# Performance work log

Hardware: AMD Instinct MI355X
Metric: run time of the kernel (lower is better)

The kernel has to match this reference:

```python
import jax, jax.numpy as jnp
import numpy as np
from jax import lax

D_MODEL, D_INNER, D_CONV, DT_RANK, D_STATE = 1024, 2048, 4, 64, 16
B_SZ, L = 1, 2048
EPS = 1e-5


def setup_inputs() -> dict:
    key = jax.random.key(0)
    ks = jax.random.split(key, 10)
    s = 0.02
    return {
        "x": jax.random.normal(ks[0], (B_SZ, L, D_MODEL), dtype=jnp.float32),
        "W_in": jax.random.normal(ks[1], (2 * D_INNER, D_MODEL), dtype=jnp.float32) * s,
        "conv_w": jax.random.normal(ks[2], (D_INNER, D_CONV), dtype=jnp.float32) * 0.1,
        "conv_b": jnp.zeros((D_INNER,), dtype=jnp.float32),
        "W_xproj": jax.random.normal(ks[3], (DT_RANK + 2 * D_STATE, D_INNER), dtype=jnp.float32) * s,
        "W_dt": jax.random.normal(ks[4], (D_INNER, DT_RANK), dtype=jnp.float32) * s,
        "b_dt": jnp.zeros((D_INNER,), dtype=jnp.float32),
        "A_log": jnp.broadcast_to(jnp.log(jnp.arange(1, D_STATE + 1, dtype=jnp.float32)), (D_INNER, D_STATE)).copy(),
        "D": jnp.ones((D_INNER,), dtype=jnp.float32),
        "W_out": jax.random.normal(ks[5], (D_MODEL, D_INNER), dtype=jnp.float32) * s,
        "norm_w": jnp.ones((D_MODEL,), dtype=jnp.float32),
    }


def _mamba_block(xn, W_in, conv_w, conv_b, W_xproj, W_dt, b_dt, A_log, D, W_out):
    b, l, _ = xn.shape
    # in_proj -> split into x branch and gate (res) branch
    xz = jnp.einsum("bld,ed->ble", xn, W_in)  # (b, l, 2*d_inner)
    xc, res = jnp.split(xz, 2, axis=-1)
    # depthwise causal conv1d over time (padding=d_conv-1, trimmed to l)
    xp = jnp.pad(xc, ((0, 0), (D_CONV - 1, 0), (0, 0)))
    conv = conv_b
    acc = jnp.zeros_like(xc)
    for k in range(D_CONV):
        acc = acc + xp[:, k:k + l, :] * conv_w[:, k]
    xs = jax.nn.silu(acc + conv_b)  # (b, l, d_inner)
    # x_proj -> delta (low-rank), B, C
    dbc = jnp.einsum("bld,ed->ble", xs, W_xproj)
    dt, Bm, Cm = jnp.split(dbc, [DT_RANK, DT_RANK + D_STATE], axis=-1)
    delta = jax.nn.softplus(jnp.einsum("blr,dr->bld", dt, W_dt) + b_dt)  # (b,l,d_inner)
    A = -jnp.exp(A_log)  # (d_inner, d_state)
    # discretize
    deltaA = jnp.exp(jnp.einsum("bld,dn->bldn", delta, A))
    dBu = jnp.einsum("bld,bln,bld->bldn", delta, Bm, xs)
    # selective scan over time
    def step(h, inp):
        dA_t, dBu_t, C_t = inp
        h = dA_t * h + dBu_t                      # (b, d_inner, d_state)
        y_t = jnp.einsum("bdn,bn->bd", h, C_t)
        return h, y_t
    h0 = jnp.zeros((b, D_INNER, D_STATE), dtype=xs.dtype)
    _, ys = lax.scan(step, h0, (deltaA.transpose(1, 0, 2, 3), dBu.transpose(1, 0, 2, 3), Cm.transpose(1, 0, 2)))
    y = ys.transpose(1, 0, 2) + xs * D  # (b, l, d_inner)
    y = y * jax.nn.silu(res)            # gate
    return jnp.einsum("bld,ed->ble", y, W_out)


def reference(x, W_in, conv_w, conv_b, W_xproj, W_dt, b_dt, A_log, D, W_out, norm_w):
    # RMSNorm
    xn = x * jax.lax.rsqrt(jnp.mean(x * x, axis=-1, keepdims=True) + EPS) * norm_w
    # Mamba mixer + residual
    return _mamba_block(xn, W_in, conv_w, conv_b, W_xproj, W_dt, b_dt, A_log, D, W_out) + x
```

## Files before the change

kernel.cpp:

```cpp
#include <hip/hip_runtime.h>
#include <hip/hip_bf16.h>

#define D_MODEL 1024
#define D_INNER 2048
#define DT_RANK 64
#define D_STATE 16
#define LSEQ    2048
#define CHUNK   32
#define NCHUNK  (LSEQ / CHUNK)
#define DN      (D_INNER * D_STATE)
#define KSPL_O  4
#define KSPL_X  16

typedef __attribute__((ext_vector_type(8))) short  short8;
typedef __attribute__((ext_vector_type(4))) float  float4v;
typedef __hip_bfloat16 bf16;

static __device__ __forceinline__ float b2f(bf16 v) { return __bfloat162float(v); }
static __device__ __forceinline__ bf16  f2b(float v) { return __float2bfloat16(v); }
static __device__ __forceinline__ float us2f(unsigned short u) {
    union { unsigned int i; float f; } cc; cc.i = ((unsigned int)u) << 16; return cc.f;
}
static __device__ __forceinline__ unsigned short f2us(float v) {
    return __bfloat16_as_ushort(__float2bfloat16(v));
}

#define GLOAD_LDS16(g, l)                                                          \
    __builtin_amdgcn_global_load_lds((const __attribute__((address_space(1))) void*)(g), \
                                     (__attribute__((address_space(3))) void*)(l), 16, 0, 0)

#define N1 (2 * D_INNER * D_MODEL)
#define N2 (D_MODEL * D_INNER)
#define N3 (96 * D_INNER)
#define N4 (D_INNER * DT_RANK)
#define NCAST4 ((N1 + N2 + N3 + N4) / 4)
__global__ __launch_bounds__(256)
void prep_kernel(const float* __restrict__ x, const float* __restrict__ nw,
                 bf16* __restrict__ xn,
                 const float* __restrict__ w_in, const float* __restrict__ w_out,
                 const float* __restrict__ w_xp, const float* __restrict__ w_dt,
                 bf16* __restrict__ o_in, bf16* __restrict__ o_out,
                 bf16* __restrict__ o_xp, bf16* __restrict__ o_dt) {
    int t = threadIdx.x;
    if (blockIdx.x < LSEQ) {
        int l = blockIdx.x;
        float4v v = ((const float4v*)(x + (size_t)l * D_MODEL))[t];
        float ssq = v[0]*v[0] + v[1]*v[1] + v[2]*v[2] + v[3]*v[3];
        for (int o = 32; o > 0; o >>= 1) ssq += __shfl_down(ssq, o);
        __shared__ float part[4];
        int lane = t & 63, wid = t >> 6;
        if (lane == 0) part[wid] = ssq;
        __syncthreads();
        float tot = part[0] + part[1] + part[2] + part[3];
        float sc = rsqrtf(tot * (1.0f / D_MODEL) + 1e-5f);
        float4v nv = ((const float4v*)nw)[t];
        bf16* op = xn + (size_t)l * D_MODEL + t * 4;
        op[0] = f2b(v[0] * sc * nv[0]);
        op[1] = f2b(v[1] * sc * nv[1]);
        op[2] = f2b(v[2] * sc * nv[2]);
        op[3] = f2b(v[3] * sc * nv[3]);
        return;
    }
    int i4 = (blockIdx.x - LSEQ) * 256 + t;
    if (i4 >= NCAST4) return;
    const float* src; bf16* dst; int base;
    if (i4 < N1 / 4)                { src = w_in;  dst = o_in;  base = 0; }
    else if (i4 < (N1 + N2) / 4)    { src = w_out; dst = o_out; base = N1 / 4; }
    else if (i4 < (N1+N2+N3) / 4)   { src = w_xp;  dst = o_xp;  base = (N1+N2) / 4; }
    else                            { src = w_dt;  dst = o_dt;  base = (N1+N2+N3) / 4; }
    int j = i4 - base;
    float4v v = ((const float4v*)src)[j];
    bf16* o = dst + j * 4;
    o[0] = f2b(v[0]); o[1] = f2b(v[1]); o[2] = f2b(v[2]); o[3] = f2b(v[3]);
}

template <int MODE>
__global__ __launch_bounds__(512)
void gemm_fast(const bf16* __restrict__ Ab, const bf16* __restrict__ Bb,
               int M, int N, int K, int kLen,
               float* __restrict__ outF, bf16* __restrict__ outB,
               const float* __restrict__ bias) {
    __shared__ short As[2][128 * 64];
    __shared__ short Bs[2][128 * 64];
    const short* Ap = (const short*)Ab;
    const short* Bp = (const short*)Bb;

    int t = threadIdx.x;
    int lane = t & 63, wid = t >> 6;

    int bx, by, bz;
    if (MODE == 0) {
        int id = blockIdx.y * gridDim.x + blockIdx.x;
        int xcd = id & 7, slot = id >> 3;
        bx = (xcd & 3) * 8 + (slot & 7);
        by = (xcd >> 2) * 8 + (slot >> 3);
        bz = 0;
    } else if (MODE == 4) {
        int id = (blockIdx.z * gridDim.y + blockIdx.y) * gridDim.x + blockIdx.x;
        int xcd = id & 7, slot = id >> 3;
        bx = slot % gridDim.x;
        int byz = xcd * ((gridDim.y * gridDim.z) / 8) + slot / gridDim.x;
        by = byz % gridDim.y;
        bz = byz / gridDim.y;
    } else {
        bx = blockIdx.x; by = blockIdx.y; bz = blockIdx.z;
    }
    int mBase = by * 128, nBase = bx * 128;
    int kBase = bz * kLen;
    int wm = 32 * (wid >> 1), wn = 64 * (wid & 1);
    int lr = lane & 15, quad = lane >> 4;

    int srow = 16 * wid + (lane >> 3);
    int cg2 = (lane & 7) ^ (lane >> 3);
    const short* gA = Ap + (size_t)(mBase + srow) * K + cg2 * 8;
    const short* gB = Bp + (size_t)(nBase + srow) * K + cg2 * 8;

    float4v acc[2][4] = {};

    #pragma unroll
    for (int g = 0; g < 2; ++g) {
        GLOAD_LDS16(gA + (size_t)g * 8 * K + kBase, &As[0][(16 * wid + g * 8) * 64]);
        GLOAD_LDS16(gB + (size_t)g * 8 * K + kBase, &Bs[0][(16 * wid + g * 8) * 64]);
    }

    int p = 0;
    for (int kt = kBase; kt < kBase + kLen; kt += 64, p ^= 1) {
        __syncthreads();
        if (kt + 64 < kBase + kLen) {
            int kn = kt + 64, q = p ^ 1;
            #pragma unroll
            for (int g = 0; g < 2; ++g) {
                GLOAD_LDS16(gA + (size_t)g * 8 * K + kn, &As[q][(16 * wid + g * 8) * 64]);
                GLOAD_LDS16(gB + (size_t)g * 8 * K + kn, &Bs[q][(16 * wid + g * 8) * 64]);
            }
        }
        #pragma unroll
        for (int s = 0; s < 2; ++s) {
            short8 af[2], bfr[4];
            #pragma unroll
            for (int i = 0; i < 2; ++i) {
                int row = wm + i * 16 + lr;
                af[i] = *(const short8*)&As[p][row * 64 + (((s * 4 + quad) ^ (lr & 7)) * 8)];
            }
            #pragma unroll
            for (int j = 0; j < 4; ++j) {
                int row = wn + j * 16 + lr;
                bfr[j] = *(const short8*)&Bs[p][row * 64 + (((s * 4 + quad) ^ (lr & 7)) * 8)];
            }
            #pragma unroll
            for (int i = 0; i < 2; ++i)
                #pragma unroll
                for (int j = 0; j < 4; ++j)
                    acc[i][j] = __builtin_amdgcn_mfma_f32_16x16x32_bf16(af[i], bfr[j], acc[i][j], 0, 0, 0);
        }
    }

    #pragma unroll
    for (int i = 0; i < 2; ++i) {
        #pragma unroll
        for (int j = 0; j < 4; ++j) {
            #pragma unroll
            for (int r = 0; r < 4; ++r) {
                int gm = mBase + wm + i * 16 + quad * 4 + r;
                int gn = nBase + wn + j * 16 + lr;
                float v = acc[i][j][r];
                if (MODE == 0) {
                    outB[(size_t)gm * N + gn] = f2b(v);
                } else if (MODE == 2) {
                    v += bias[gn];
                    v = (v > 20.0f) ? v : log1pf(__expf(v));
                    outB[(size_t)gm * N + gn] = f2b(v);
                } else {
                    outF[((size_t)bz * M + gm) * N + gn] = v;
                }
            }
        }
    }
}

__global__ __launch_bounds__(128)
void reduce_xproj(const float* __restrict__ part, float* __restrict__ dbc,
                  bf16* __restrict__ dtb) {
    int m = blockIdx.x, j = threadIdx.x;
    if (j >= 96) return;
    float v = 0.0f;
    #pragma unroll
    for (int z = 0; z < KSPL_X; ++z)
        v += part[((size_t)z * LSEQ + m) * 128 + j];
    dbc[(size_t)m * 96 + j] = v;
    if (j < DT_RANK) dtb[(size_t)m * DT_RANK + j] = f2b(v);
}

__global__ __launch_bounds__(256)
void reduce_out(const float* __restrict__ part, const float* __restrict__ x,
                float* __restrict__ out) {
    int i = blockIdx.x * 256 + threadIdx.x;
    const int MN4 = LSEQ * D_MODEL / 4;
    float4v a = ((const float4v*)part)[i];
    #pragma unroll
    for (int z = 1; z < KSPL_O; ++z) {
        float4v b = ((const float4v*)part)[(size_t)z * MN4 + i];
        a[0] += b[0]; a[1] += b[1]; a[2] += b[2]; a[3] += b[3];
    }
    float4v xv = ((const float4v*)x)[i];
    a[0] += xv[0]; a[1] += xv[1]; a[2] += xv[2]; a[3] += xv[3];
    ((float4v*)out)[i] = a;
}

__global__ void conv_kernel(const bf16* __restrict__ xz, const float* __restrict__ cw,
                            const float* __restrict__ cb, bf16* __restrict__ xsb) {
    int idx = blockIdx.x * 256 + threadIdx.x;
    int c = (idx & (D_INNER / 2 - 1)) * 2;
    int l0 = (idx >> 10) * 4;
    float4v wA = ((const float4v*)cw)[c];
    float4v wB = ((const float4v*)cw)[c + 1];
    float bA = cb[c], bB = cb[c + 1];
    const unsigned int* col = (const unsigned int*)((const unsigned short*)xz + c);
    float vA[7], vB[7];
    #pragma unroll
    for (int j = 0; j < 7; ++j) {
        int l = l0 - 3 + j;
        if (l >= 0) {
            unsigned int u = col[(size_t)l * D_INNER];
            vA[j] = us2f((unsigned short)(u & 0xffff));
            vB[j] = us2f((unsigned short)(u >> 16));
        } else { vA[j] = 0.0f; vB[j] = 0.0f; }
    }
    #pragma unroll
    for (int j = 0; j < 4; ++j) {
        float aA = bA + vA[j]*wA[0] + vA[j+1]*wA[1] + vA[j+2]*wA[2] + vA[j+3]*wA[3];
        float aB = bB + vB[j]*wB[0] + vB[j+1]*wB[1] + vB[j+2]*wB[2] + vB[j+3]*wB[3];
        float sA = aA * (1.0f / (1.0f + __expf(-aA)));
        float sB = aB * (1.0f / (1.0f + __expf(-aB)));
        unsigned int o = (unsigned int)f2us(sA) | ((unsigned int)f2us(sB) << 16);
        *(unsigned int*)((unsigned short*)xsb + (size_t)(l0 + j) * D_INNER + c) = o;
    }
}

template <int PASS>
__global__ __launch_bounds__(256)
void scan2(const bf16* __restrict__ delta, const bf16* __restrict__ xsb,
           const float* __restrict__ dbc, const bf16* __restrict__ xz,
           const float* __restrict__ A_log, const float* __restrict__ Dw,
           const float* __restrict__ Hinit,
           float* __restrict__ P, float* __restrict__ S, bf16* __restrict__ yg) {
    __shared__ float bc[CHUNK][32];
    int t = threadIdx.x;
    int d = blockIdx.x * 256 + t;
    int c = blockIdx.y;
    int l0 = c * CHUNK;

    {
        int row = t >> 3, col = (t & 7) * 4;
        *(float4v*)&bc[row][col] = *(const float4v*)&dbc[(size_t)(l0 + row) * 96 + 64 + col];
    }
    __syncthreads();

    float A[16], h[16], pr[16];
    #pragma unroll
    for (int n = 0; n < 16; ++n) A[n] = -__expf(A_log[(size_t)d * 16 + n]);
    if (PASS == 0) {
        #pragma unroll
        for (int n = 0; n < 16; ++n) { h[n] = 0.0f; pr[n] = 1.0f; }
    } else {
        #pragma unroll
        for (int n = 0; n < 16; n += 4)
            *(float4v*)&h[n] = *(const float4v*)&Hinit[(size_t)c * DN + (size_t)d * 16 + n];
    }
    float Dd = (PASS == 1) ? Dw[d] : 0.0f;

    for (int i = 0; i < CHUNK; ++i) {
        int l = l0 + i;
        float dv = b2f(delta[(size_t)l * D_INNER + d]);
        float xv = b2f(xsb[(size_t)l * D_INNER + d]);
        float u = dv * xv;
        #pragma unroll
        for (int n = 0; n < 16; ++n) {
            float a = __expf(dv * A[n]);
            h[n] = fmaf(a, h[n], bc[i][n] * u);
            if (PASS == 0) pr[n] *= a;
        }
        if (PASS == 1) {
            float y = xv * Dd;
            #pragma unroll
            for (int n = 0; n < 16; ++n) y = fmaf(h[n], bc[i][16 + n], y);
            float r = b2f(xz[(size_t)l * (2 * D_INNER) + D_INNER + d]);
            float g = r * (1.0f / (1.0f + __expf(-r)));
            yg[(size_t)l * D_INNER + d] = f2b(y * g);
        }
    }
    if (PASS == 0) {
        #pragma unroll
        for (int n = 0; n < 16; n += 4) {
            *(float4v*)&P[(size_t)c * DN + (size_t)d * 16 + n] = *(float4v*)&pr[n];
            *(float4v*)&S[(size_t)c * DN + (size_t)d * 16 + n] = *(float4v*)&h[n];
        }
    }
}

__global__ __launch_bounds__(256)
void scan_mid(const float* __restrict__ P, const float* __restrict__ S,
              float* __restrict__ Hinit) {
    int idx = blockIdx.x * 256 + threadIdx.x;
    float h = 0.0f;
    for (int c0 = 0; c0 < NCHUNK; c0 += 8) {
        float p[8], s[8];
        #pragma unroll
        for (int j = 0; j < 8; ++j) {
            p[j] = P[(size_t)(c0 + j) * DN + idx];
            s[j] = S[(size_t)(c0 + j) * DN + idx];
        }
        #pragma unroll
        for (int j = 0; j < 8; ++j) {
            Hinit[(size_t)(c0 + j) * DN + idx] = h;
            h = fmaf(p[j], h, s[j]);
        }
    }
}

extern "C" void kernel_launch(void* const* d_in, const int* in_sizes, int n_in,
                              void* d_out, int out_size, void* d_ws, size_t ws_size,
                              hipStream_t stream) {
    const float* x       = (const float*)d_in[0];
    const float* W_in    = (const float*)d_in[1];
    const float* conv_w  = (const float*)d_in[2];
    const float* conv_b  = (const float*)d_in[3];
    const float* W_xproj = (const float*)d_in[4];
    const float* W_dt    = (const float*)d_in[5];
    const float* b_dt    = (const float*)d_in[6];
    const float* A_log   = (const float*)d_in[7];
    const float* Dw      = (const float*)d_in[8];
    const float* W_out   = (const float*)d_in[9];
    const float* norm_w  = (const float*)d_in[10];

    char* w = (char*)d_ws;
    bf16* W_in_b    = (bf16*)w; w += (size_t)2 * D_INNER * D_MODEL * 2;
    bf16* W_out_b   = (bf16*)w; w += (size_t)D_MODEL * D_INNER * 2;
    bf16* W_xproj_b = (bf16*)w; w += (size_t)128 * D_INNER * 2;
    bf16* W_dt_b    = (bf16*)w; w += (size_t)D_INNER * DT_RANK * 2;
    char* reuse0 = w;
    bf16* xn        = (bf16*)w; w += (size_t)LSEQ * D_MODEL * 2;
    bf16* xz        = (bf16*)w; w += (size_t)LSEQ * 2 * D_INNER * 2;
    bf16* xsb       = (bf16*)w; w += (size_t)LSEQ * D_INNER * 2;
    bf16* delta     = (bf16*)w; w += (size_t)LSEQ * D_INNER * 2;
    float* dbc      = (float*)w; w += (size_t)LSEQ * 96 * 4;
    bf16* dtb       = (bf16*)w; w += (size_t)LSEQ * DT_RANK * 2;
    bf16* yg        = (bf16*)w; w += (size_t)LSEQ * D_INNER * 2;
    float* Pbuf     = (float*)w; w += (size_t)NCHUNK * DN * 4;
    float* Sbuf     = (float*)w; w += (size_t)NCHUNK * DN * 4;
    float* Hinit    = (float*)w; w += (size_t)NCHUNK * DN * 4;
    float* xp_part  = (float*)w; w += (size_t)KSPL_X * LSEQ * 128 * 4;
    float* out_part = (float*)reuse0;

    prep_kernel<<<LSEQ + (NCAST4 + 255) / 256, 256, 0, stream>>>(
        x, norm_w, xn, W_in, W_out, W_xproj, W_dt, W_in_b, W_out_b, W_xproj_b, W_dt_b);

    gemm_fast<0><<<dim3(4096 / 128, 2048 / 128, 1), 512, 0, stream>>>(
        xn, W_in_b, 2048, 4096, 1024, 1024, nullptr, xz, nullptr);

    conv_kernel<<<(LSEQ / 4) * (D_INNER / 2) / 256, 256, 0, stream>>>(xz, conv_w, conv_b, xsb);

    gemm_fast<4><<<dim3(1, 2048 / 128, KSPL_X), 512, 0, stream>>>(
        xsb, W_xproj_b, 2048, 128, 2048, 2048 / KSPL_X, xp_part, nullptr, nullptr);
    reduce_xproj<<<LSEQ, 128, 0, stream>>>(xp_part, dbc, dtb);

    gemm_fast<2><<<dim3(2048 / 128, 2048 / 128, 1), 512, 0, stream>>>(
        dtb, W_dt_b, 2048, 2048, 64, 64, nullptr, delta, b_dt);

    dim3 sgrid(D_INNER / 256, NCHUNK);
    scan2<0><<<sgrid, 256, 0, stream>>>(delta, xsb, dbc, xz, A_log, Dw,
                                        nullptr, Pbuf, Sbuf, nullptr);
    scan_mid<<<DN / 256, 256, 0, stream>>>(Pbuf, Sbuf, Hinit);
    scan2<1><<<sgrid, 256, 0, stream>>>(delta, xsb, dbc, xz, A_log, Dw,
                                        Hinit, nullptr, nullptr, yg);

    gemm_fast<4><<<dim3(1024 / 128, 2048 / 128, KSPL_O), 512, 0, stream>>>(
        yg, W_out_b, 2048, 1024, 2048, 2048 / KSPL_O, out_part, nullptr, nullptr);
    reduce_out<<<LSEQ * D_MODEL / 4 / 256, 256, 0, stream>>>(out_part, x, (float*)d_out);
}
```

Measured before the change: 248.4 us.

## Store out-proj split-K partials in bf16 and drop XCD block remapping

The out-projection split-K GEMM now writes its partial sums as bf16 instead of fp32 through a new MODE 5, and reduce_out reads and accumulates those bf16 partials. The aim is to halve the partial-buffer write and read traffic. Separately, the XCD-aware block-index swizzle for MODE 0 and MODE 4 is removed and plain blockIdx is used, which may reduce L2 locality. Rounding partials to bf16 before the reduction adds precision loss.

```diff
diff --git a/kernel.cpp b/kernel.cpp
--- a/kernel.cpp
+++ b/kernel.cpp
@@ -13,6 +13,7 @@
 #define KSPL_X  16
 
 typedef __attribute__((ext_vector_type(8))) short  short8;
+typedef __attribute__((ext_vector_type(4))) short  short4v;
 typedef __attribute__((ext_vector_type(4))) float  float4v;
 typedef __hip_bfloat16 bf16;
 
@@ -87,26 +88,8 @@
 
     int t = threadIdx.x;
     int lane = t & 63, wid = t >> 6;
-
-    int bx, by, bz;
-    if (MODE == 0) {
-        int id = blockIdx.y * gridDim.x + blockIdx.x;
-        int xcd = id & 7, slot = id >> 3;
-        bx = (xcd & 3) * 8 + (slot & 7);
-        by = (xcd >> 2) * 8 + (slot >> 3);
-        bz = 0;
-    } else if (MODE == 4) {
-        int id = (blockIdx.z * gridDim.y + blockIdx.y) * gridDim.x + blockIdx.x;
-        int xcd = id & 7, slot = id >> 3;
-        bx = slot % gridDim.x;
-        int byz = xcd * ((gridDim.y * gridDim.z) / 8) + slot / gridDim.x;
-        by = byz % gridDim.y;
-        bz = byz / gridDim.y;
-    } else {
-        bx = blockIdx.x; by = blockIdx.y; bz = blockIdx.z;
-    }
-    int mBase = by * 128, nBase = bx * 128;
-    int kBase = bz * kLen;
+    int mBase = blockIdx.y * 128, nBase = blockIdx.x * 128;
+    int kBase = blockIdx.z * kLen;
     int wm = 32 * (wid >> 1), wn = 64 * (wid & 1);
     int lr = lane & 15, quad = lane >> 4;
 
@@ -170,8 +153,10 @@
                     v += bias[gn];
                     v = (v > 20.0f) ? v : log1pf(__expf(v));
                     outB[(size_t)gm * N + gn] = f2b(v);
+                } else if (MODE == 4) {
+                    outF[((size_t)blockIdx.z * M + gm) * N + gn] = v;
                 } else {
-                    outF[((size_t)bz * M + gm) * N + gn] = v;
+                    outB[((size_t)blockIdx.z * M + gm) * N + gn] = f2b(v);
                 }
             }
         }
@@ -192,19 +177,22 @@
 }
 
 __global__ __launch_bounds__(256)
-void reduce_out(const float* __restrict__ part, const float* __restrict__ x,
+void reduce_out(const bf16* __restrict__ part, const float* __restrict__ x,
                 float* __restrict__ out) {
     int i = blockIdx.x * 256 + threadIdx.x;
-    const int MN4 = LSEQ * D_MODEL / 4;
-    float4v a = ((const float4v*)part)[i];
-    #pragma unroll
-    for (int z = 1; z < KSPL_O; ++z) {
-        float4v b = ((const float4v*)part)[(size_t)z * MN4 + i];
-        a[0] += b[0]; a[1] += b[1]; a[2] += b[2]; a[3] += b[3];
+    const size_t MN = (size_t)LSEQ * D_MODEL;
+    float a0 = 0, a1 = 0, a2 = 0, a3 = 0;
+    #pragma unroll
+    for (int z = 0; z < KSPL_O; ++z) {
+        short4v b = *(const short4v*)((const short*)part + z * MN + (size_t)i * 4);
+        a0 += us2f((unsigned short)b[0]);
+        a1 += us2f((unsigned short)b[1]);
+        a2 += us2f((unsigned short)b[2]);
+        a3 += us2f((unsigned short)b[3]);
     }
     float4v xv = ((const float4v*)x)[i];
-    a[0] += xv[0]; a[1] += xv[1]; a[2] += xv[2]; a[3] += xv[3];
-    ((float4v*)out)[i] = a;
+    float4v o = {a0 + xv[0], a1 + xv[1], a2 + xv[2], a3 + xv[3]};
+    ((float4v*)out)[i] = o;
 }
 
 __global__ void conv_kernel(const bf16* __restrict__ xz, const float* __restrict__ cw,
@@ -350,7 +338,7 @@
     float* Sbuf     = (float*)w; w += (size_t)NCHUNK * DN * 4;
     float* Hinit    = (float*)w; w += (size_t)NCHUNK * DN * 4;
     float* xp_part  = (float*)w; w += (size_t)KSPL_X * LSEQ * 128 * 4;
-    float* out_part = (float*)reuse0;
+    bf16* out_part  = (bf16*)reuse0;
 
     prep_kernel<<<LSEQ + (NCAST4 + 255) / 256, 256, 0, stream>>>(
         x, norm_w, xn, W_in, W_out, W_xproj, W_dt, W_in_b, W_out_b, W_xproj_b, W_dt_b);
@@ -374,7 +362,7 @@
     scan2<1><<<sgrid, 256, 0, stream>>>(delta, xsb, dbc, xz, A_log, Dw,
                                         Hinit, nullptr, nullptr, yg);
 
-    gemm_fast<4><<<dim3(1024 / 128, 2048 / 128, KSPL_O), 512, 0, stream>>>(
-        yg, W_out_b, 2048, 1024, 2048, 2048 / KSPL_O, out_part, nullptr, nullptr);
+    gemm_fast<5><<<dim3(1024 / 128, 2048 / 128, KSPL_O), 512, 0, stream>>>(
+        yg, W_out_b, 2048, 1024, 2048, 2048 / KSPL_O, nullptr, out_part, nullptr);
     reduce_out<<<LSEQ * D_MODEL / 4 / 256, 256, 0, stream>>>(out_part, x, (float*)d_out);
 }
```

New measurement: 241.0 us. -3.0%, faster.
